# Kernel tuning notes

Measured on AMD Instinct MI355X. Metric: run time of the kernel, lower is better.

## Reference

```python
import jax, jax.numpy as jnp
import numpy as np

N_PER, B, DEG = 1000, 20, 32
N = N_PER * B            # 20000 nodes
D_IN, D_OUT = 128, 128
K_PER = 50
ASSIGN = K_PER * B       # 1000 clusters total (block-diagonal per graph)
E = N_PER * DEG * B      # 640000 edges


def setup_inputs() -> dict:
    key = jax.random.key(0)
    k1, k2, k3, k4 = jax.random.split(key, 4)
    h = jax.random.normal(k1, (N, D_IN), dtype=jnp.float32)
    W_feat = jax.random.normal(k2, (2 * D_IN, D_OUT), dtype=jnp.float32) * 0.05
    b_feat = jnp.zeros((D_OUT,), jnp.float32)
    W_pool = jax.random.normal(k3, (2 * D_IN, ASSIGN), dtype=jnp.float32) * 0.05
    b_pool = jnp.zeros((ASSIGN,), jnp.float32)
    # block-structured edges: each graph's edges stay within its node range
    e = jax.random.randint(k4, (B, N_PER * DEG, 2), 0, N_PER)
    e = e + (jnp.arange(B) * N_PER)[:, None, None]
    e = e.reshape(-1, 2)
    src = e[:, 0].astype(jnp.int32)
    dst = e[:, 1].astype(jnp.int32)
    # block-diagonal assignment mask (scipy.linalg.block_diag of ones blocks)
    gid_node = jnp.repeat(jnp.arange(B), N_PER)   # graph id of each node
    gid_col = jnp.repeat(jnp.arange(B), K_PER)    # graph id of each cluster col
    mask = (gid_node[:, None] == gid_col[None, :]).astype(jnp.float32)
    return dict(h=h, W_feat=W_feat, b_feat=b_feat, W_pool=W_pool,
                b_pool=b_pool, src=src, dst=dst, mask=mask)


def _graphsage(h, src, dst, W, b):
    # mean aggregator over incoming edges: c[d] = mean_{(s,d) in E} h[s]
    msum = jax.ops.segment_sum(h[src], dst, num_segments=N)
    cnt = jax.ops.segment_sum(jnp.ones((src.shape[0], 1), h.dtype), dst,
                              num_segments=N)
    c = msum / jnp.maximum(cnt, 1.0)
    # Bundler: Linear(cat(h, c)) -> L2 normalize -> activation
    z = jnp.concatenate([h, c], axis=1) @ W + b
    z = z / jnp.maximum(jnp.linalg.norm(z, axis=1, keepdims=True), 1e-12)
    return jax.nn.relu(z)


def reference(h, W_feat, b_feat, W_pool, b_pool, src, dst, mask):
    feat = _graphsage(h, src, dst, W_feat, b_feat)        # [N, D_OUT]
    assign = _graphsage(h, src, dst, W_pool, b_pool)      # [N, ASSIGN]
    # masked_softmax (memory_efficient=False, allennlp-style)
    p = jax.nn.softmax(assign * mask, axis=-1)
    p = p * mask
    p = p / (jnp.sum(p, axis=-1, keepdims=True) + 1e-13)  # [N, ASSIGN]
    h_pool = p.T @ feat                                   # [ASSIGN, D_OUT]
    # sparse A @ S, with A[dst, src] = 1 per edge (DGL adjacency convention)
    a_s = jax.ops.segment_sum(p[src], dst, num_segments=N)  # [N, ASSIGN]
    adj_new = p.T @ a_s                                     # [ASSIGN, ASSIGN]
    return adj_new, h_pool
```

## Files before the change

### kernel.cpp

```cpp
#include <hip/hip_runtime.h>

#define NN 20000
#define NPG 1000
#define NBG 20
#define DD 128
#define KK2 256
#define KPC 50
#define KPAD 64
#define NAC 1000
#define NACP 1024
#define NPGP 1024
#define NNT 20480
#define NEDGE 640000
#define CAP 96
#define OUTSZ 1128000

typedef __attribute__((ext_vector_type(8))) short bfrag;
typedef __attribute__((ext_vector_type(4))) float f32x4;
typedef __attribute__((ext_vector_type(8))) unsigned short ushort8;
typedef __attribute__((ext_vector_type(8))) _Float16 half8;

__device__ __forceinline__ unsigned short f2bf(float f) {
  unsigned int u = __builtin_bit_cast(unsigned int, f);
  unsigned int r = (u + 0x7FFFu + ((u >> 16) & 1u)) >> 16;
  return (unsigned short)r;
}
__device__ __forceinline__ float bf2f(unsigned short u) {
  return __builtin_bit_cast(float, ((unsigned int)u) << 16);
}

__device__ __forceinline__ int xcd_swz(int orig, int nwg) {
  int q = nwg >> 3, r = nwg & 7;
  int x = orig & 7, idx = orig >> 3;
  return (x < r) ? (x * (q + 1) + idx) : (r * (q + 1) + (x - r) * q + idx);
}

__global__ __launch_bounds__(256) void k_zero(int* __restrict__ deg) {
  int idx = blockIdx.x * 256 + threadIdx.x;
  if (idx < 5000) ((int4*)deg)[idx] = make_int4(0, 0, 0, 0);
}

__global__ __launch_bounds__(256) void k_prep(
    const float* __restrict__ h, const float* __restrict__ Wf,
    const float* __restrict__ Wp, const float* __restrict__ bp,
    const int* __restrict__ src, const int* __restrict__ dst,
    int* __restrict__ deg, int* __restrict__ ssrc,
    unsigned short* __restrict__ xb,
    unsigned short* __restrict__ Wtp, unsigned short* __restrict__ Wtf,
    unsigned short* __restrict__ Wpb,
    float* __restrict__ v, float* __restrict__ bb,
    unsigned short* __restrict__ pT, float* __restrict__ out) {
  __shared__ float red[256];
  int b = blockIdx.x;
  int tid = threadIdx.x;
  if (b < 2500) {
    int e = b * 256 + tid;
    if (e < NEDGE) {
      int d = dst[e];
      int pos = atomicAdd(&deg[d], 1);
      ssrc[d * CAP + pos] = src[e];
    }
  } else if (b < 3750) {
    int idx = (b - 2500) * 256 + tid;
    int n = idx >> 4, seg = idx & 15;
    const float4* hp = (const float4*)(h + n * DD + seg * 8);
    float4 x0 = hp[0], x1 = hp[1];
    ushort8 o;
    o[0] = f2bf(x0.x); o[1] = f2bf(x0.y); o[2] = f2bf(x0.z); o[3] = f2bf(x0.w);
    o[4] = f2bf(x1.x); o[5] = f2bf(x1.y); o[6] = f2bf(x1.z); o[7] = f2bf(x1.w);
    *(ushort8*)(xb + n * KK2 + seg * 8) = o;
  } else if (b < 4006) {
    int wid = tid >> 6, lane = tid & 63;
    int col = (b - 3750) * 4 + wid;
    #pragma unroll
    for (int i = 0; i < 4; ++i) {
      int kk = i * 64 + lane;
      float val = (col < NAC) ? Wp[kk * NAC + col] : 0.f;
      Wtp[col * KK2 + kk] = f2bf(val);
    }
  } else if (b < 4038) {
    int wid = tid >> 6, lane = tid & 63;
    int col = (b - 4006) * 4 + wid;
    #pragma unroll
    for (int i = 0; i < 4; ++i) {
      int kk = i * 64 + lane;
      Wtf[col * KK2 + kk] = f2bf(Wf[kk * DD + col]);
    }
  } else if (b < 4166) {
    int idx = (b - 4038) * 256 + tid;
    int rrow = idx >> 7;
    int seg = idx & 127;
    ushort8 o;
    #pragma unroll
    for (int i = 0; i < 8; ++i) {
      int cc = seg * 8 + i;
      o[i] = (cc < NAC) ? f2bf(Wp[rrow * NAC + cc]) : (unsigned short)0;
    }
    *(ushort8*)(Wpb + rrow * NACP + seg * 8) = o;
  } else if (b < 4422) {
    int i = b - 4166;
    float acc = 0.f;
    for (int k = tid; k < NAC; k += 256) acc += Wp[i * NAC + k] * bp[k];
    red[tid] = acc;
    __syncthreads();
    for (int st = 128; st > 0; st >>= 1) {
      if (tid < st) red[tid] += red[tid + st];
      __syncthreads();
    }
    if (tid == 0) v[i] = red[0];
    if (i == 0) {
      __syncthreads();
      float a2 = 0.f;
      for (int k = tid; k < NAC; k += 256) { float t = bp[k]; a2 += t * t; }
      red[tid] = a2;
      __syncthreads();
      for (int st = 128; st > 0; st >>= 1) {
        if (tid < st) red[tid] += red[tid + st];
        __syncthreads();
      }
      if (tid == 0) *bb = red[0];
    }
  } else if (b < 5062) {
    int idx = (b - 4422) * 256 + tid;
    ((int4*)pT)[idx] = make_int4(0, 0, 0, 0);
  } else {
    int idx = (b - 5062) * 256 + tid;
    if (idx < OUTSZ / 4) ((float4*)out)[idx] = make_float4(0.f, 0.f, 0.f, 0.f);
  }
}

__global__ __launch_bounds__(256) void k_mid(
    const unsigned short* __restrict__ Wpb, unsigned short* __restrict__ Gb,
    const int* __restrict__ deg, const int* __restrict__ ssrc,
    unsigned short* __restrict__ xb) {
  int b = blockIdx.x;
  int tid = threadIdx.x;
  if (b < 16) {
    int i0 = (b & 3) * 64, j0 = (b >> 2) * 64;
    int wid = tid >> 6, lane = tid & 63;
    int lr = lane & 15, lg = lane >> 4;
    f32x4 acc[4] = {};
    for (int kt = 0; kt < 32; ++kt) {
      bfrag a[4], bfr;
      #pragma unroll
      for (int m = 0; m < 4; ++m)
        a[m] = *reinterpret_cast<const bfrag*>(Wpb + (size_t)(i0 + m * 16 + lr) * NACP + kt * 32 + lg * 8);
      bfr = *reinterpret_cast<const bfrag*>(Wpb + (size_t)(j0 + wid * 16 + lr) * NACP + kt * 32 + lg * 8);
      #pragma unroll
      for (int m = 0; m < 4; ++m)
        acc[m] = __builtin_amdgcn_mfma_f32_16x16x32_bf16(a[m], bfr, acc[m], 0, 0, 0);
    }
    #pragma unroll
    for (int m = 0; m < 4; ++m)
      #pragma unroll
      for (int r = 0; r < 4; ++r) {
        int row = i0 + m * 16 + lg * 4 + r;
        int col = j0 + wid * 16 + lr;
        Gb[row * 256 + col] = f2bf(acc[m][r]);
      }
  } else {
    int wg = xcd_swz(b - 16, 1250);
    int node = wg * 16 + (tid >> 4);
    int lane = tid & 15;
    int dg = deg[node];
    const int* sl = ssrc + node * CAP;
    float a[8] = {};
    int j = 0;
    for (; j + 8 <= dg; j += 8) {
      int4 ia = *(const int4*)&sl[j];
      int4 ib = *(const int4*)&sl[j + 4];
      ushort8 w0 = *(const ushort8*)(xb + (size_t)ia.x * KK2 + lane * 8);
      ushort8 w1 = *(const ushort8*)(xb + (size_t)ia.y * KK2 + lane * 8);
      ushort8 w2 = *(const ushort8*)(xb + (size_t)ia.z * KK2 + lane * 8);
      ushort8 w3 = *(const ushort8*)(xb + (size_t)ia.w * KK2 + lane * 8);
      ushort8 w4 = *(const ushort8*)(xb + (size_t)ib.x * KK2 + lane * 8);
      ushort8 w5 = *(const ushort8*)(xb + (size_t)ib.y * KK2 + lane * 8);
      ushort8 w6 = *(const ushort8*)(xb + (size_t)ib.z * KK2 + lane * 8);
      ushort8 w7 = *(const ushort8*)(xb + (size_t)ib.w * KK2 + lane * 8);
      #pragma unroll
      for (int i = 0; i < 8; ++i)
        a[i] += ((bf2f(w0[i]) + bf2f(w1[i])) + (bf2f(w2[i]) + bf2f(w3[i]))) +
                ((bf2f(w4[i]) + bf2f(w5[i])) + (bf2f(w6[i]) + bf2f(w7[i])));
    }
    for (; j + 4 <= dg; j += 4) {
      int4 idx = *(const int4*)&sl[j];
      ushort8 v0 = *(const ushort8*)(xb + (size_t)idx.x * KK2 + lane * 8);
      ushort8 v1 = *(const ushort8*)(xb + (size_t)idx.y * KK2 + lane * 8);
      ushort8 v2 = *(const ushort8*)(xb + (size_t)idx.z * KK2 + lane * 8);
      ushort8 v3 = *(const ushort8*)(xb + (size_t)idx.w * KK2 + lane * 8);
      #pragma unroll
      for (int i = 0; i < 8; ++i)
        a[i] += bf2f(v0[i]) + bf2f(v1[i]) + bf2f(v2[i]) + bf2f(v3[i]);
    }
    for (; j < dg; ++j) {
      ushort8 vv = *(const ushort8*)(xb + (size_t)sl[j] * KK2 + lane * 8);
      #pragma unroll
      for (int i = 0; i < 8; ++i) a[i] += bf2f(vv[i]);
    }
    float inv = 1.f / (float)max(dg, 1);
    ushort8 o;
    #pragma unroll
    for (int i = 0; i < 8; ++i) o[i] = f2bf(a[i] * inv);
    *(ushort8*)(xb + node * KK2 + DD + lane * 8) = o;
  }
}

__global__ __launch_bounds__(256) void k_fused(
    const unsigned short* __restrict__ xb, const unsigned short* __restrict__ Gb,
    const unsigned short* __restrict__ Wtp,
    const float* __restrict__ bp,
    const float* __restrict__ v, const float* __restrict__ bbp,
    _Float16* __restrict__ p_pad, unsigned short* __restrict__ pT) {
  __shared__ int4 xs4[1024];
  __shared__ float zbuf[32][52];
  __shared__ float nrm_lds[32];
  int n0 = blockIdx.x * 32;
  int tid = threadIdx.x;
  for (int i = tid; i < 1024; i += 256) {
    int row = i >> 5;
    xs4[i ^ (row & 7)] = ((const int4*)xb)[(size_t)(n0 + row) * 32 + (i & 31)];
  }
  if (tid < 32) nrm_lds[tid] = 0.f;
  __syncthreads();

  int wid = tid >> 6, lane = tid & 63;
  int lr = lane & 15, lg = lane >> 4;
  const unsigned short* xsu = (const unsigned short*)xs4;

  {
    f32x4 accy[2][4] = {};
    #pragma unroll
    for (int kt = 0; kt < 8; ++kt) {
      bfrag a[2], bfr[4];
      #pragma unroll
      for (int m = 0; m < 2; ++m) {
        int slot = (m * 16 + lr) * 32 + kt * 4 + lg;
        a[m] = *reinterpret_cast<const bfrag*>(&xs4[slot ^ ((slot >> 5) & 7)]);
      }
      #pragma unroll
      for (int c = 0; c < 4; ++c) {
        int j = wid * 64 + c * 16 + lr;
        bfr[c] = *reinterpret_cast<const bfrag*>(Gb + (size_t)j * KK2 + kt * 32 + lg * 8);
      }
      #pragma unroll
      for (int m = 0; m < 2; ++m)
        #pragma unroll
        for (int c = 0; c < 4; ++c)
          accy[m][c] = __builtin_amdgcn_mfma_f32_16x16x32_bf16(a[m], bfr[c], accy[m][c], 0, 0, 0);
    }
    float vv[4];
    #pragma unroll
    for (int c = 0; c < 4; ++c) vv[c] = v[wid * 64 + c * 16 + lr];
    #pragma unroll
    for (int m = 0; m < 2; ++m)
      #pragma unroll
      for (int r = 0; r < 4; ++r) {
        int row = m * 16 + lg * 4 + r;
        float part = 0.f;
        #pragma unroll
        for (int c = 0; c < 4; ++c) {
          int k = wid * 64 + c * 16 + lr;
          int slot = row * 32 + (k >> 3);
          float xv = bf2f(xsu[(size_t)(slot ^ (row & 7)) * 8 + (k & 7)]);
          part += (accy[m][c][r] + 2.f * vv[c]) * xv;
        }
        part += __shfl_xor(part, 1); part += __shfl_xor(part, 2);
        part += __shfl_xor(part, 4); part += __shfl_xor(part, 8);
        if (lr == 0) atomicAdd(&nrm_lds[row], part);
      }
  }

  {
    int g0 = n0 / NPG;
    int g1 = (n0 + 31) / NPG;
    for (int gp = g0; gp <= g1; ++gp) {
      int wb = gp * KPC;
      f32x4 accw[2] = {};
      #pragma unroll
      for (int kt = 0; kt < 8; ++kt) {
        bfrag a[2], bfr;
        #pragma unroll
        for (int m = 0; m < 2; ++m) {
          int slot = (m * 16 + lr) * 32 + kt * 4 + lg;
          a[m] = *reinterpret_cast<const bfrag*>(&xs4[slot ^ ((slot >> 5) & 7)]);
        }
        bfr = *reinterpret_cast<const bfrag*>(Wtp + (size_t)(wb + wid * 16 + lr) * KK2 + kt * 32 + lg * 8);
        #pragma unroll
        for (int m = 0; m < 2; ++m)
          accw[m] = __builtin_amdgcn_mfma_f32_16x16x32_bf16(a[m], bfr, accw[m], 0, 0, 0);
      }
      int wc = wid * 16 + lr;
      float bias = (wc < KPC) ? bp[wb + wc] : 0.f;
      #pragma unroll
      for (int m = 0; m < 2; ++m)
        #pragma unroll
        for (int r = 0; r < 4; ++r) {
          int row = m * 16 + lg * 4 + r;
          if (wc < KPC && (n0 + row) / NPG == gp)
            zbuf[row][wc] = accw[m][r] + bias;
        }
    }
  }
  __syncthreads();

  if (tid < 128) {
    int node = tid >> 2, q = tid & 3;
    float nv = nrm_lds[node] + bbp[0];
    float inv = 1.f / fmaxf(sqrtf(fmaxf(nv, 0.f)), 1e-12f);
    float e[16];
    float mx = -1e30f;
    #pragma unroll
    for (int i = 0; i < 16; ++i) {
      int cc = q * 16 + i;
      float sv = (cc < KPC) ? fmaxf(zbuf[node][cc] * inv, 0.f) : -1e30f;
      e[i] = sv;
      mx = fmaxf(mx, sv);
    }
    mx = fmaxf(mx, __shfl_xor(mx, 1));
    mx = fmaxf(mx, __shfl_xor(mx, 2));
    float esum = 0.f;
    #pragma unroll
    for (int i = 0; i < 16; ++i) {
      int cc = q * 16 + i;
      float ev = (cc < KPC) ? __expf(e[i] - mx) : 0.f;
      e[i] = ev;
      esum += ev;
    }
    esum += __shfl_xor(esum, 1);
    esum += __shfl_xor(esum, 2);
    float isum = 1.f / esum;
    int n = n0 + node;
    int gg = n / NPG;
    int nloc = n - gg * NPG;
    half8 o0, o1;
    #pragma unroll
    for (int i = 0; i < 8; ++i) {
      o0[i] = (_Float16)(e[i] * isum);
      o1[i] = (_Float16)(e[i + 8] * isum);
    }
    *(half8*)&p_pad[(size_t)n * KPAD + q * 16] = o0;
    *(half8*)&p_pad[(size_t)n * KPAD + q * 16 + 8] = o1;
    #pragma unroll
    for (int i = 0; i < 16; ++i) {
      int cc = q * 16 + i;
      pT[((size_t)gg * KPAD + cc) * NPGP + nloc] = f2bf(e[i] * isum);
    }
  }
}

__global__ __launch_bounds__(256) void k_as(
    const _Float16* __restrict__ p_pad, const int* __restrict__ deg,
    const int* __restrict__ ssrc, unsigned short* __restrict__ asT,
    const unsigned short* __restrict__ xb, const unsigned short* __restrict__ Wtf,
    const float* __restrict__ bfeat, unsigned short* __restrict__ featT) {
  __shared__ int4 big[2048];
  __shared__ float nrmf[64];
  int b = blockIdx.x;
  int tid = threadIdx.x;
  if (b < 625) {
    unsigned short* as_lds = (unsigned short*)big;
    int wg = xcd_swz(b, 625);
    int nrow = tid >> 3;
    int n = wg * 32 + nrow;
    int lane = tid & 7;
    int dg = deg[n];
    const int* sl = ssrc + n * CAP;
    float a[8] = {};
    int j = 0;
    for (; j + 8 <= dg; j += 8) {
      int4 ia = *(const int4*)&sl[j];
      int4 ib = *(const int4*)&sl[j + 4];
      half8 w0 = *(const half8*)(p_pad + (size_t)ia.x * KPAD + lane * 8);
      half8 w1 = *(const half8*)(p_pad + (size_t)ia.y * KPAD + lane * 8);
      half8 w2 = *(const half8*)(p_pad + (size_t)ia.z * KPAD + lane * 8);
      half8 w3 = *(const half8*)(p_pad + (size_t)ia.w * KPAD + lane * 8);
      half8 w4 = *(const half8*)(p_pad + (size_t)ib.x * KPAD + lane * 8);
      half8 w5 = *(const half8*)(p_pad + (size_t)ib.y * KPAD + lane * 8);
      half8 w6 = *(const half8*)(p_pad + (size_t)ib.z * KPAD + lane * 8);
      half8 w7 = *(const half8*)(p_pad + (size_t)ib.w * KPAD + lane * 8);
      #pragma unroll
      for (int i = 0; i < 8; ++i)
        a[i] += (((float)w0[i] + (float)w1[i]) + ((float)w2[i] + (float)w3[i])) +
                (((float)w4[i] + (float)w5[i]) + ((float)w6[i] + (float)w7[i]));
    }
    for (; j + 4 <= dg; j += 4) {
      int4 idx = *(const int4*)&sl[j];
      half8 v0 = *(const half8*)(p_pad + (size_t)idx.x * KPAD + lane * 8);
      half8 v1 = *(const half8*)(p_pad + (size_t)idx.y * KPAD + lane * 8);
      half8 v2 = *(const half8*)(p_pad + (size_t)idx.z * KPAD + lane * 8);
      half8 v3 = *(const half8*)(p_pad + (size_t)idx.w * KPAD + lane * 8);
      #pragma unroll
      for (int i = 0; i < 8; ++i)
        a[i] += (float)v0[i] + (float)v1[i] + (float)v2[i] + (float)v3[i];
    }
    for (; j < dg; ++j) {
      half8 vv = *(const half8*)(p_pad + (size_t)sl[j] * KPAD + lane * 8);
      #pragma unroll
      for (int i = 0; i < 8; ++i) a[i] += (float)vv[i];
    }
    #pragma unroll
    for (int i = 0; i < 8; ++i)
      as_lds[(lane * 8 + i) * 40 + nrow] = f2bf(a[i]);
    __syncthreads();
    {
      int col = tid >> 2, off = (tid & 3) * 8;
      *(ushort8*)(asT + (size_t)col * NNT + wg * 32 + off) = *(const ushort8*)&as_lds[col * 40 + off];
    }
  } else {
    int n0 = (b - 625) * 64;
    int nt = min(64, NN - n0);
    for (int i = tid; i < 2048; i += 256) {
      int row = i >> 5;
      int4 vv = make_int4(0, 0, 0, 0);
      if (row < nt) vv = ((const int4*)xb)[(size_t)(n0 + row) * 32 + (i & 31)];
      big[i ^ (row & 7)] = vv;
    }
    if (tid < 64) nrmf[tid] = 0.f;
    __syncthreads();
    int wid = tid >> 6, lane = tid & 63;
    int lr = lane & 15, lg = lane >> 4;
    f32x4 acc[4][2] = {};
    #pragma unroll
    for (int kt = 0; kt < 8; ++kt) {
      bfrag a[4], bfr[2];
      #pragma unroll
      for (int m = 0; m < 4; ++m) {
        int slot = (m * 16 + lr) * 32 + kt * 4 + lg;
        a[m] = *reinterpret_cast<const bfrag*>(&big[slot ^ ((slot >> 5) & 7)]);
      }
      #pragma unroll
      for (int c = 0; c < 2; ++c) {
        int col = wid * 32 + c * 16 + lr;
        bfr[c] = *reinterpret_cast<const bfrag*>(Wtf + (size_t)col * KK2 + kt * 32 + lg * 8);
      }
      #pragma unroll
      for (int m = 0; m < 4; ++m)
        #pragma unroll
        for (int c = 0; c < 2; ++c)
          acc[m][c] = __builtin_amdgcn_mfma_f32_16x16x32_bf16(a[m], bfr[c], acc[m][c], 0, 0, 0);
    }
    float nf[4][4] = {};
    #pragma unroll
    for (int c = 0; c < 2; ++c) {
      int col = wid * 32 + c * 16 + lr;
      float bias = bfeat[col];
      #pragma unroll
      for (int m = 0; m < 4; ++m)
        #pragma unroll
        for (int r = 0; r < 4; ++r) {
          float z = acc[m][c][r] + bias;
          acc[m][c][r] = z;
          nf[m][r] += z * z;
        }
    }
    #pragma unroll
    for (int m = 0; m < 4; ++m)
      #pragma unroll
      for (int r = 0; r < 4; ++r) {
        float p = nf[m][r];
        p += __shfl_xor(p, 1); p += __shfl_xor(p, 2);
        p += __shfl_xor(p, 4); p += __shfl_xor(p, 8);
        if (lr == 0) atomicAdd(&nrmf[m * 16 + lg * 4 + r], p);
      }
    __syncthreads();
    unsigned short* ftl = (unsigned short*)big;
    #pragma unroll
    for (int m = 0; m < 4; ++m)
      #pragma unroll
      for (int r = 0; r < 4; ++r) {
        int row = m * 16 + lg * 4 + r;
        float sc = 1.f / fmaxf(sqrtf(nrmf[row]), 1e-12f);
        #pragma unroll
        for (int c = 0; c < 2; ++c) {
          int col = wid * 32 + c * 16 + lr;
          ftl[col * 72 + row] = f2bf(fmaxf(acc[m][c][r] * sc, 0.f));
        }
      }
    __syncthreads();
    #pragma unroll
    for (int p2 = 0; p2 < 4; ++p2) {
      int c2 = tid + p2 * 256;
      int col = c2 >> 3, off = (c2 & 7) * 8;
      if (n0 + off < NN)
        *(ushort8*)(featT + (size_t)col * NNT + n0 + off) = *(const ushort8*)&ftl[col * 72 + off];
    }
  }
}

__global__ __launch_bounds__(256) void k_final(
    const unsigned short* __restrict__ pT, const unsigned short* __restrict__ featT,
    const unsigned short* __restrict__ asT, float* __restrict__ out) {
  int g = blockIdx.x >> 3;
  int kc = blockIdx.x & 7;
  int tid = threadIdx.x;
  int wid = tid >> 6, lane = tid & 63;
  int lr = lane & 15, lg = lane >> 4;
  f32x4 acc[3][4] = {};
  const unsigned short* bbase[3];
  #pragma unroll
  for (int j = 0; j < 3; ++j) {
    int cf = wid * 3 + j;
    bbase[j] = (cf < 8) ? (featT + (size_t)(cf * 16 + lr) * NNT)
                        : (asT + (size_t)((cf - 8) * 16 + lr) * NNT);
  }
  int nb0 = g * NPG + kc * 128;
  #pragma unroll
  for (int ks = 0; ks < 4; ++ks) {
    bfrag a[4], bfr[3];
    #pragma unroll
    for (int m = 0; m < 4; ++m)
      a[m] = *(const bfrag*)(pT + ((size_t)g * KPAD + m * 16 + lr) * NPGP + kc * 128 + ks * 32 + lg * 8);
    #pragma unroll
    for (int j = 0; j < 3; ++j)
      bfr[j] = *(const bfrag*)(bbase[j] + nb0 + ks * 32 + lg * 8);
    #pragma unroll
    for (int j = 0; j < 3; ++j)
      #pragma unroll
      for (int m = 0; m < 4; ++m)
        acc[j][m] = __builtin_amdgcn_mfma_f32_16x16x32_bf16(a[m], bfr[j], acc[j][m], 0, 0, 0);
  }
  #pragma unroll
  for (int j = 0; j < 3; ++j) {
    int cf = wid * 3 + j;
    #pragma unroll
    for (int m = 0; m < 4; ++m)
      #pragma unroll
      for (int r = 0; r < 4; ++r) {
        int i = m * 16 + lg * 4 + r;
        if (i < KPC) {
          if (cf < 8) {
            int col = cf * 16 + lr;
            atomicAdd(&out[1000000 + (size_t)(g * KPC + i) * DD + col], acc[j][m][r]);
          } else {
            int col2 = (cf - 8) * 16 + lr;
            if (col2 < KPC)
              atomicAdd(&out[(size_t)(g * KPC + i) * NAC + g * KPC + col2], acc[j][m][r]);
          }
        }
      }
  }
}

extern "C" void kernel_launch(void* const* d_in, const int* in_sizes, int n_in,
                              void* d_out, int out_size, void* d_ws, size_t ws_size,
                              hipStream_t stream) {
  const float* h = (const float*)d_in[0];
  const float* Wf = (const float*)d_in[1];
  const float* bf = (const float*)d_in[2];
  const float* Wp = (const float*)d_in[3];
  const float* bp = (const float*)d_in[4];
  const int* src = (const int*)d_in[5];
  const int* dst = (const int*)d_in[6];
  float* out = (float*)d_out;
  char* ws = (char*)d_ws;

  int* deg = (int*)(ws + 0);
  int* ssrc = (int*)(ws + 80000);
  unsigned short* xb = (unsigned short*)(ws + 7760000);
  _Float16* p_pad = (_Float16*)(ws + 18000000);
  unsigned short* featT = (unsigned short*)(ws + 20560000);
  unsigned short* asT = (unsigned short*)(ws + 25802880);
  unsigned short* Wpb = (unsigned short*)(ws + 28424320);
  unsigned short* Gb = (unsigned short*)(ws + 28948608);
  float* v = (float*)(ws + 29079680);
  float* bb = (float*)(ws + 29080704);
  unsigned short* Wtp = (unsigned short*)(ws + 29081728);
  unsigned short* Wtf = (unsigned short*)(ws + 29606016);
  unsigned short* pT = (unsigned short*)(ws + 29671552);

  k_zero<<<20, 256, 0, stream>>>(deg);
  k_prep<<<6164, 256, 0, stream>>>(h, Wf, Wp, bp, src, dst, deg, ssrc, xb, Wtp, Wtf, Wpb, v, bb, pT, out);
  k_mid<<<1266, 256, 0, stream>>>(Wpb, Gb, deg, ssrc, xb);
  k_fused<<<625, 256, 0, stream>>>(xb, Gb, Wtp, bp, v, bb, p_pad, pT);
  k_as<<<938, 256, 0, stream>>>(p_pad, deg, ssrc, asT, xb, Wtf, bf, featT);
  k_final<<<160, 256, 0, stream>>>(pT, featT, asT, out);
}
```

Before: 121.0 us.

## Replace gather-based neighbor aggregation with dense block-diagonal adjacency MFMA matmuls

Edges are now accumulated as 4-bit counts into a dense per-graph adjacency matrix (1000x1024 nibbles per graph) instead of a CSR-like src list. The mean aggregation and the A@P product are then computed as bf16 MFMA matmuls against a transposed bf16 copy of h and against pT. This replaces irregular gathers with dense tensor-core work and drops the fp16 p_pad buffer. The cost is zeroing and atomically filling a roughly 10 MB count matrix, and 4-bit counts can overflow if a node receives 16 or more edges from the same source.

Measured after the change: 211.7 us. 75.0% more time.

```diff
diff --git a/kernel.cpp b/kernel.cpp
--- a/kernel.cpp
+++ b/kernel.cpp
@@ -12,13 +12,11 @@
 #define NPGP 1024
 #define NNT 20480
 #define NEDGE 640000
-#define CAP 96
 #define OUTSZ 1128000
 
 typedef __attribute__((ext_vector_type(8))) short bfrag;
 typedef __attribute__((ext_vector_type(4))) float f32x4;
 typedef __attribute__((ext_vector_type(8))) unsigned short ushort8;
-typedef __attribute__((ext_vector_type(8))) _Float16 half8;
 
 __device__ __forceinline__ unsigned short f2bf(float f) {
   unsigned int u = __builtin_bit_cast(unsigned int, f);
@@ -35,30 +33,59 @@
   return (x < r) ? (x * (q + 1) + idx) : (r * (q + 1) + (x - r) * q + idx);
 }
 
-__global__ __launch_bounds__(256) void k_zero(int* __restrict__ deg) {
-  int idx = blockIdx.x * 256 + threadIdx.x;
-  if (idx < 5000) ((int4*)deg)[idx] = make_int4(0, 0, 0, 0);
+__device__ __forceinline__ bfrag unpack_afrag(unsigned int cw, float s) {
+  bfrag af;
+  #pragma unroll
+  for (int i = 0; i < 8; ++i) {
+    float w = (float)((cw >> (4 * i)) & 0xFu) * s;
+    af[i] = (short)f2bf(w);
+  }
+  return af;
+}
+
+__global__ __launch_bounds__(256) void k_zero(int* __restrict__ deg,
+                                              unsigned int* __restrict__ Ac,
+                                              unsigned short* __restrict__ pT,
+                                              float* __restrict__ out) {
+  int b = blockIdx.x, tid = threadIdx.x;
+  if (b < 20) {
+    int idx = b * 256 + tid;
+    if (idx < 5000) ((int4*)deg)[idx] = make_int4(0, 0, 0, 0);
+  } else if (b < 2520) {
+    int idx = (b - 20) * 256 + tid;
+    ((int4*)Ac)[idx] = make_int4(0, 0, 0, 0);
+  } else if (b < 3160) {
+    int idx = (b - 2520) * 256 + tid;
+    ((int4*)pT)[idx] = make_int4(0, 0, 0, 0);
+  } else {
+    int idx = (b - 3160) * 256 + tid;
+    if (idx < OUTSZ / 4) ((float4*)out)[idx] = make_float4(0.f, 0.f, 0.f, 0.f);
+  }
 }
 
 __global__ __launch_bounds__(256) void k_prep(
     const float* __restrict__ h, const float* __restrict__ Wf,
     const float* __restrict__ Wp, const float* __restrict__ bp,
     const int* __restrict__ src, const int* __restrict__ dst,
-    int* __restrict__ deg, int* __restrict__ ssrc,
+    int* __restrict__ deg, unsigned int* __restrict__ Ac,
     unsigned short* __restrict__ xb,
     unsigned short* __restrict__ Wtp, unsigned short* __restrict__ Wtf,
     unsigned short* __restrict__ Wpb,
     float* __restrict__ v, float* __restrict__ bb,
-    unsigned short* __restrict__ pT, float* __restrict__ out) {
+    unsigned short* __restrict__ hT) {
+  __shared__ int4 big[2048];
   __shared__ float red[256];
   int b = blockIdx.x;
   int tid = threadIdx.x;
   if (b < 2500) {
     int e = b * 256 + tid;
     if (e < NEDGE) {
-      int d = dst[e];
-      int pos = atomicAdd(&deg[d], 1);
-      ssrc[d * CAP + pos] = src[e];
+      int d = dst[e], s = src[e];
+      atomicAdd(&deg[d], 1);
+      int g = d / NPG;
+      int sl = s - g * NPG;
+      size_t nib = (size_t)d * NACP + sl;
+      atomicAdd(&Ac[nib >> 3], 1u << ((nib & 7) * 4));
     }
   } else if (b < 3750) {
     int idx = (b - 2500) * 256 + tid;
@@ -120,25 +147,38 @@
       }
       if (tid == 0) *bb = red[0];
     }
-  } else if (b < 5062) {
-    int idx = (b - 4422) * 256 + tid;
-    ((int4*)pT)[idx] = make_int4(0, 0, 0, 0);
   } else {
-    int idx = (b - 5062) * 256 + tid;
-    if (idx < OUTSZ / 4) ((float4*)out)[idx] = make_float4(0.f, 0.f, 0.f, 0.f);
-  }
-}
-
-__global__ __launch_bounds__(256) void k_mid(
+    int n0 = (b - 4422) * 64;
+    unsigned short* ltr = (unsigned short*)big;
+    for (int i = tid; i < 2048; i += 256) {
+      int node = i >> 5, off = i & 31;
+      float4 vv = make_float4(0.f, 0.f, 0.f, 0.f);
+      if (n0 + node < NN) vv = ((const float4*)h)[(size_t)(n0 + node) * 32 + off];
+      ltr[(off * 4 + 0) * 72 + node] = f2bf(vv.x);
+      ltr[(off * 4 + 1) * 72 + node] = f2bf(vv.y);
+      ltr[(off * 4 + 2) * 72 + node] = f2bf(vv.z);
+      ltr[(off * 4 + 3) * 72 + node] = f2bf(vv.w);
+    }
+    __syncthreads();
+    #pragma unroll
+    for (int p2 = 0; p2 < 4; ++p2) {
+      int c2 = tid + p2 * 256;
+      int dim = c2 >> 3, off = (c2 & 7) * 8;
+      *(ushort8*)(hT + (size_t)dim * NNT + n0 + off) = *(const ushort8*)&ltr[dim * 72 + off];
+    }
+  }
+}
+
+__global__ __launch_bounds__(256) void k_agg(
     const unsigned short* __restrict__ Wpb, unsigned short* __restrict__ Gb,
-    const int* __restrict__ deg, const int* __restrict__ ssrc,
-    unsigned short* __restrict__ xb) {
+    const unsigned int* __restrict__ Ac, const int* __restrict__ deg,
+    const unsigned short* __restrict__ hT, unsigned short* __restrict__ xb) {
   int b = blockIdx.x;
   int tid = threadIdx.x;
+  int wid = tid >> 6, lane = tid & 63;
+  int lr = lane & 15, lg = lane >> 4;
   if (b < 16) {
     int i0 = (b & 3) * 64, j0 = (b >> 2) * 64;
-    int wid = tid >> 6, lane = tid & 63;
-    int lr = lane & 15, lg = lane >> 4;
     f32x4 acc[4] = {};
     for (int kt = 0; kt < 32; ++kt) {
       bfrag a[4], bfr;
@@ -159,49 +199,31 @@
         Gb[row * 256 + col] = f2bf(acc[m][r]);
       }
   } else {
-    int wg = xcd_swz(b - 16, 1250);
-    int node = wg * 16 + (tid >> 4);
-    int lane = tid & 15;
-    int dg = deg[node];
-    const int* sl = ssrc + node * CAP;
-    float a[8] = {};
-    int j = 0;
-    for (; j + 8 <= dg; j += 8) {
-      int4 ia = *(const int4*)&sl[j];
-      int4 ib = *(const int4*)&sl[j + 4];
-      ushort8 w0 = *(const ushort8*)(xb + (size_t)ia.x * KK2 + lane * 8);
-      ushort8 w1 = *(const ushort8*)(xb + (size_t)ia.y * KK2 + lane * 8);
-      ushort8 w2 = *(const ushort8*)(xb + (size_t)ia.z * KK2 + lane * 8);
-      ushort8 w3 = *(const ushort8*)(xb + (size_t)ia.w * KK2 + lane * 8);
-      ushort8 w4 = *(const ushort8*)(xb + (size_t)ib.x * KK2 + lane * 8);
-      ushort8 w5 = *(const ushort8*)(xb + (size_t)ib.y * KK2 + lane * 8);
-      ushort8 w6 = *(const ushort8*)(xb + (size_t)ib.z * KK2 + lane * 8);
-      ushort8 w7 = *(const ushort8*)(xb + (size_t)ib.w * KK2 + lane * 8);
-      #pragma unroll
-      for (int i = 0; i < 8; ++i)
-        a[i] += ((bf2f(w0[i]) + bf2f(w1[i])) + (bf2f(w2[i]) + bf2f(w3[i]))) +
-                ((bf2f(w4[i]) + bf2f(w5[i])) + (bf2f(w6[i]) + bf2f(w7[i])));
-    }
-    for (; j + 4 <= dg; j += 4) {
-      int4 idx = *(const int4*)&sl[j];
-      ushort8 v0 = *(const ushort8*)(xb + (size_t)idx.x * KK2 + lane * 8);
-      ushort8 v1 = *(const ushort8*)(xb + (size_t)idx.y * KK2 + lane * 8);
-      ushort8 v2 = *(const ushort8*)(xb + (size_t)idx.z * KK2 + lane * 8);
-      ushort8 v3 = *(const ushort8*)(xb + (size_t)idx.w * KK2 + lane * 8);
-      #pragma unroll
-      for (int i = 0; i < 8; ++i)
-        a[i] += bf2f(v0[i]) + bf2f(v1[i]) + bf2f(v2[i]) + bf2f(v3[i]);
-    }
-    for (; j < dg; ++j) {
-      ushort8 vv = *(const ushort8*)(xb + (size_t)sl[j] * KK2 + lane * 8);
-      #pragma unroll
-      for (int i = 0; i < 8; ++i) a[i] += bf2f(vv[i]);
-    }
-    float inv = 1.f / (float)max(dg, 1);
-    ushort8 o;
-    #pragma unroll
-    for (int i = 0; i < 8; ++i) o[i] = f2bf(a[i] * inv);
-    *(ushort8*)(xb + node * KK2 + DD + lane * 8) = o;
+    int wg = xcd_swz(b - 16, 320);
+    int g = wg >> 4, t = wg & 15;
+    int dl = t * 64 + wid * 16 + lr;
+    int dgi = min(g * NPG + min(dl, NPG - 1), NN - 1);
+    float invd = 1.f / (float)max(deg[dgi], 1);
+    const unsigned int* arow = Ac + (size_t)(g * NPG + dl) * 128;
+    f32x4 acc[8] = {};
+    for (int kt = 0; kt < 32; ++kt) {
+      bfrag af = unpack_afrag(arow[kt * 4 + lg], invd);
+      #pragma unroll
+      for (int cf = 0; cf < 8; ++cf) {
+        bfrag bfr = *(const bfrag*)(hT + (size_t)(cf * 16 + lr) * NNT + g * NPG + kt * 32 + lg * 8);
+        acc[cf] = __builtin_amdgcn_mfma_f32_16x16x32_bf16(af, bfr, acc[cf], 0, 0, 0);
+      }
+    }
+    int dbase = t * 64 + wid * 16 + lg * 4;
+    #pragma unroll
+    for (int r = 0; r < 4; ++r) {
+      int dls = dbase + r;
+      if (dls < NPG) {
+        #pragma unroll
+        for (int cf = 0; cf < 8; ++cf)
+          xb[(size_t)(g * NPG + dls) * KK2 + DD + cf * 16 + lr] = f2bf(acc[cf][r]);
+      }
+    }
   }
 }
 
@@ -210,7 +232,7 @@
     const unsigned short* __restrict__ Wtp,
     const float* __restrict__ bp,
     const float* __restrict__ v, const float* __restrict__ bbp,
-    _Float16* __restrict__ p_pad, unsigned short* __restrict__ pT) {
+    unsigned short* __restrict__ pT) {
   __shared__ int4 xs4[1024];
   __shared__ float zbuf[32][52];
   __shared__ float nrm_lds[32];
@@ -332,14 +354,6 @@
     int n = n0 + node;
     int gg = n / NPG;
     int nloc = n - gg * NPG;
-    half8 o0, o1;
-    #pragma unroll
-    for (int i = 0; i < 8; ++i) {
-      o0[i] = (_Float16)(e[i] * isum);
-      o1[i] = (_Float16)(e[i + 8] * isum);
-    }
-    *(half8*)&p_pad[(size_t)n * KPAD + q * 16] = o0;
-    *(half8*)&p_pad[(size_t)n * KPAD + q * 16 + 8] = o1;
     #pragma unroll
     for (int i = 0; i < 16; ++i) {
       int cc = q * 16 + i;
@@ -348,66 +362,47 @@
   }
 }
 
-__global__ __launch_bounds__(256) void k_as(
-    const _Float16* __restrict__ p_pad, const int* __restrict__ deg,
-    const int* __restrict__ ssrc, unsigned short* __restrict__ asT,
+__global__ __launch_bounds__(256) void k_as2(
+    const unsigned int* __restrict__ Ac,
+    const unsigned short* __restrict__ pT, unsigned short* __restrict__ asT,
     const unsigned short* __restrict__ xb, const unsigned short* __restrict__ Wtf,
     const float* __restrict__ bfeat, unsigned short* __restrict__ featT) {
   __shared__ int4 big[2048];
   __shared__ float nrmf[64];
   int b = blockIdx.x;
   int tid = threadIdx.x;
-  if (b < 625) {
-    unsigned short* as_lds = (unsigned short*)big;
-    int wg = xcd_swz(b, 625);
-    int nrow = tid >> 3;
-    int n = wg * 32 + nrow;
-    int lane = tid & 7;
-    int dg = deg[n];
-    const int* sl = ssrc + n * CAP;
-    float a[8] = {};
-    int j = 0;
-    for (; j + 8 <= dg; j += 8) {
-      int4 ia = *(const int4*)&sl[j];
-      int4 ib = *(const int4*)&sl[j + 4];
-      half8 w0 = *(const half8*)(p_pad + (size_t)ia.x * KPAD + lane * 8);
-      half8 w1 = *(const half8*)(p_pad + (size_t)ia.y * KPAD + lane * 8);
-      half8 w2 = *(const half8*)(p_pad + (size_t)ia.z * KPAD + lane * 8);
-      half8 w3 = *(const half8*)(p_pad + (size_t)ia.w * KPAD + lane * 8);
-      half8 w4 = *(const half8*)(p_pad + (size_t)ib.x * KPAD + lane * 8);
-      half8 w5 = *(const half8*)(p_pad + (size_t)ib.y * KPAD + lane * 8);
-      half8 w6 = *(const half8*)(p_pad + (size_t)ib.z * KPAD + lane * 8);
-      half8 w7 = *(const half8*)(p_pad + (size_t)ib.w * KPAD + lane * 8);
-      #pragma unroll
-      for (int i = 0; i < 8; ++i)
-        a[i] += (((float)w0[i] + (float)w1[i]) + ((float)w2[i] + (float)w3[i])) +
-                (((float)w4[i] + (float)w5[i]) + ((float)w6[i] + (float)w7[i]));
-    }
-    for (; j + 4 <= dg; j += 4) {
-      int4 idx = *(const int4*)&sl[j];
-      half8 v0 = *(const half8*)(p_pad + (size_t)idx.x * KPAD + lane * 8);
-      half8 v1 = *(const half8*)(p_pad + (size_t)idx.y * KPAD + lane * 8);
-      half8 v2 = *(const half8*)(p_pad + (size_t)idx.z * KPAD + lane * 8);
-      half8 v3 = *(const half8*)(p_pad + (size_t)idx.w * KPAD + lane * 8);
-      #pragma unroll
-      for (int i = 0; i < 8; ++i)
-        a[i] += (float)v0[i] + (float)v1[i] + (float)v2[i] + (float)v3[i];
-    }
-    for (; j < dg; ++j) {
-      half8 vv = *(const half8*)(p_pad + (size_t)sl[j] * KPAD + lane * 8);
-      #pragma unroll
-      for (int i = 0; i < 8; ++i) a[i] += (float)vv[i];
-    }
-    #pragma unroll
-    for (int i = 0; i < 8; ++i)
-      as_lds[(lane * 8 + i) * 40 + nrow] = f2bf(a[i]);
+  int wid = tid >> 6, lane = tid & 63;
+  int lr = lane & 15, lg = lane >> 4;
+  if (b < 320) {
+    int wg = xcd_swz(b, 320);
+    int g = wg >> 4, t = wg & 15;
+    int dl = t * 64 + wid * 16 + lr;
+    const unsigned int* arow = Ac + (size_t)(g * NPG + dl) * 128;
+    f32x4 acc[4] = {};
+    for (int kt = 0; kt < 32; ++kt) {
+      bfrag af = unpack_afrag(arow[kt * 4 + lg], 1.0f);
+      #pragma unroll
+      for (int cf = 0; cf < 4; ++cf) {
+        bfrag bfr = *(const bfrag*)(pT + ((size_t)g * KPAD + cf * 16 + lr) * NPGP + kt * 32 + lg * 8);
+        acc[cf] = __builtin_amdgcn_mfma_f32_16x16x32_bf16(af, bfr, acc[cf], 0, 0, 0);
+      }
+    }
+    unsigned short* as_l = (unsigned short*)big;
+    #pragma unroll
+    for (int cf = 0; cf < 4; ++cf)
+      #pragma unroll
+      for (int r = 0; r < 4; ++r)
+        as_l[(cf * 16 + lr) * 72 + wid * 16 + lg * 4 + r] = f2bf(acc[cf][r]);
     __syncthreads();
-    {
-      int col = tid >> 2, off = (tid & 3) * 8;
-      *(ushort8*)(asT + (size_t)col * NNT + wg * 32 + off) = *(const ushort8*)&as_lds[col * 40 + off];
+    #pragma unroll
+    for (int p2 = 0; p2 < 2; ++p2) {
+      int c2 = tid + p2 * 256;
+      int col = c2 >> 3, off = (c2 & 7) * 8;
+      if (t * 64 + off < NPG)
+        *(ushort8*)(asT + (size_t)col * NNT + g * NPG + t * 64 + off) = *(const ushort8*)&as_l[col * 72 + off];
     }
   } else {
-    int n0 = (b - 625) * 64;
+    int n0 = (b - 320) * 64;
     int nt = min(64, NN - n0);
     for (int i = tid; i < 2048; i += 256) {
       int row = i >> 5;
@@ -417,8 +412,6 @@
     }
     if (tid < 64) nrmf[tid] = 0.f;
     __syncthreads();
-    int wid = tid >> 6, lane = tid & 63;
-    int lr = lane & 15, lg = lane >> 4;
     f32x4 acc[4][2] = {};
     #pragma unroll
     for (int kt = 0; kt < 8; ++kt) {
@@ -555,10 +548,10 @@
   char* ws = (char*)d_ws;
 
   int* deg = (int*)(ws + 0);
-  int* ssrc = (int*)(ws + 80000);
-  unsigned short* xb = (unsigned short*)(ws + 7760000);
-  _Float16* p_pad = (_Float16*)(ws + 18000000);
-  unsigned short* featT = (unsigned short*)(ws + 20560000);
+  unsigned int* Ac = (unsigned int*)(ws + 80000);
+  unsigned short* xb = (unsigned short*)(ws + 10320000);
+  unsigned short* hT = (unsigned short*)(ws + 20560000);
+  unsigned short* featT = hT;
   unsigned short* asT = (unsigned short*)(ws + 25802880);
   unsigned short* Wpb = (unsigned short*)(ws + 28424320);
   unsigned short* Gb = (unsigned short*)(ws + 28948608);
@@ -568,10 +561,10 @@
   unsigned short* Wtf = (unsigned short*)(ws + 29606016);
   unsigned short* pT = (unsigned short*)(ws + 29671552);
 
-  k_zero<<<20, 256, 0, stream>>>(deg);
-  k_prep<<<6164, 256, 0, stream>>>(h, Wf, Wp, bp, src, dst, deg, ssrc, xb, Wtp, Wtf, Wpb, v, bb, pT, out);
-  k_mid<<<1266, 256, 0, stream>>>(Wpb, Gb, deg, ssrc, xb);
-  k_fused<<<625, 256, 0, stream>>>(xb, Gb, Wtp, bp, v, bb, p_pad, pT);
-  k_as<<<938, 256, 0, stream>>>(p_pad, deg, ssrc, asT, xb, Wtf, bf, featT);
+  k_zero<<<4262, 256, 0, stream>>>(deg, Ac, pT, out);
+  k_prep<<<4735, 256, 0, stream>>>(h, Wf, Wp, bp, src, dst, deg, Ac, xb, Wtp, Wtf, Wpb, v, bb, hT);
+  k_agg<<<336, 256, 0, stream>>>(Wpb, Gb, Ac, deg, hT, xb);
+  k_fused<<<625, 256, 0, stream>>>(xb, Gb, Wtp, bp, v, bb, pT);
+  k_as2<<<633, 256, 0, stream>>>(Ac, pT, asT, xb, Wtf, bf, featT);
   k_final<<<160, 256, 0, stream>>>(pT, featT, asT, out);
 }
```
